# Kernel tuning notes

Hardware: AMD Instinct MI355X
Metric: run time of the kernel (lower is better)

Reference implementation:

```python
import jax, jax.numpy as jnp
import numpy as np

B, T, C, H = 2, 2048, 2048, 16
HD = C // H  # head dim = 128


def setup_inputs() -> dict:
    key = jax.random.key(0)
    k1, k2, k3 = jax.random.split(key, 3)
    x = jax.random.normal(k1, (B, T, C), dtype=jnp.float32)
    # torch Linear stores weight as [out_features, in_features]; y = x @ W.T
    w_attn = jax.random.normal(k2, (3 * C, C), dtype=jnp.float32) * (C ** -0.5)
    w_proj = jax.random.normal(k3, (C, C), dtype=jnp.float32) * (C ** -0.5)
    b_proj = jnp.zeros((C,), dtype=jnp.float32)
    return {"x": x, "w_attn": w_attn, "w_proj": w_proj, "b_proj": b_proj}


def reference(x, w_attn, w_proj, b_proj):
    # c_attn: [B,T,C] -> [B,T,3C], then split into q,k,v
    qkv = jnp.einsum('btc,oc->bto', x, w_attn)
    q, k, v = jnp.split(qkv, 3, axis=-1)
    # [B,T,C] -> [B,H,T,HD]
    q = q.reshape(B, T, H, HD).transpose(0, 2, 1, 3)
    k = k.reshape(B, T, H, HD).transpose(0, 2, 1, 3)
    v = v.reshape(B, T, H, HD).transpose(0, 2, 1, 3)
    scale = 1.0 / jnp.sqrt(jnp.float32(HD))
    att = jnp.einsum('bhqd,bhkd->bhqk', q, k) * scale  # [B,H,T,T]
    causal = jnp.tril(jnp.ones((T, T), dtype=bool))
    att = jnp.where(causal, att, -jnp.inf)
    att = jax.nn.softmax(att, axis=-1)
    # dropout p=0.0 (eval): identity
    y = jnp.einsum('bhqk,bhkd->bhqd', att, v)  # [B,H,T,HD]
    y = y.transpose(0, 2, 1, 3).reshape(B, T, C)
    y = jnp.einsum('btc,oc->bto', y, w_proj) + b_proj
    return y
```

## Files before the change

### kernel.cpp

```cpp
#include <hip/hip_runtime.h>
#include <hip/hip_bf16.h>
#include <stdint.h>
#include <stddef.h>

#define Bn  2
#define Tn  2048
#define Cn  2048
#define Hn  16
#define HDn 128

typedef short short8   __attribute__((ext_vector_type(8)));
typedef short short8_a __attribute__((ext_vector_type(8), may_alias));
typedef unsigned int u32x4_a __attribute__((ext_vector_type(4), may_alias));
typedef unsigned short u16x4_a __attribute__((ext_vector_type(4), may_alias));
typedef unsigned short u16x8_a __attribute__((ext_vector_type(8), may_alias));
typedef float f32x4 __attribute__((ext_vector_type(4)));

typedef __attribute__((address_space(1))) const void av1_t;
typedef __attribute__((address_space(3))) void av3_t;

__device__ inline unsigned short f2b(float f) {
    union { float f; unsigned u; } v; v.f = f;
    unsigned r = v.u + 0x7fffu + ((v.u >> 16) & 1u);
    return (unsigned short)(r >> 16);
}
__device__ inline u16x4_a cvt4_f32_bf16(u32x4_a v) {
    u16x4_a h;
#pragma unroll
    for (int e = 0; e < 4; e++) {
        unsigned u = v[e];
        unsigned r = u + 0x7fffu + ((u >> 16) & 1u);
        h[e] = (unsigned short)(r >> 16);
    }
    return h;
}

__global__ __launch_bounds__(256)
void cvt_kernel(const float* __restrict__ src, unsigned short* __restrict__ dst, int n)
{
    const int i = (blockIdx.x * 256 + threadIdx.x) * 8;
    if (i >= n) return;
    u32x4_a a = *(const u32x4_a*)((const unsigned*)src + i);
    u32x4_a b = *(const u32x4_a*)((const unsigned*)src + i + 4);
    u16x8_a o;
    u16x4_a ha = cvt4_f32_bf16(a), hb = cvt4_f32_bf16(b);
#pragma unroll
    for (int e = 0; e < 4; e++) { o[e] = ha[e]; o[e + 4] = hb[e]; }
    *(u16x8_a*)(dst + i) = o;
}

template<int OUT_F32, int HAS_BIAS>
__global__ __launch_bounds__(256)
void gemm_bb_kernel(const unsigned short* __restrict__ A,
                    const unsigned short* __restrict__ Bm,
                    const float* __restrict__ bias, void* __restrict__ Cv,
                    int M, int N, int K)
{
    __shared__ __align__(16) unsigned short As[128 * 32];
    __shared__ __align__(16) unsigned short Bs[128 * 32];

    const int tid  = threadIdx.x;
    const int lane = tid & 63;
    const int wave = tid >> 6;
    const int quad = lane >> 4;
    const int l15  = lane & 15;
    const int tm = blockIdx.x * 128;
    const int tn = blockIdx.y * 128;
    const int wr = (wave >> 1) * 64;
    const int wc = (wave & 1) * 64;

    const int srow = lane >> 2;
    const int scol = (lane & 3) * 8;

    f32x4 acc[4][4];
#pragma unroll
    for (int i = 0; i < 4; i++)
#pragma unroll
        for (int j = 0; j < 4; j++) acc[i][j] = (f32x4){0.f, 0.f, 0.f, 0.f};

    const int ksteps = K >> 5;
    for (int kt = 0; kt < ksteps; ++kt) {
        const int k0 = kt << 5;
#pragma unroll
        for (int r = 0; r < 2; r++) {
            const int row = (r * 4 + wave) * 16 + srow;
            __builtin_amdgcn_global_load_lds(
                (av1_t*)(A + (size_t)(tm + row) * K + k0 + scol),
                (av3_t*)(&As[row * 32 + scol]), 16, 0, 0);
            __builtin_amdgcn_global_load_lds(
                (av1_t*)(Bm + (size_t)(tn + row) * K + k0 + scol),
                (av3_t*)(&Bs[row * 32 + scol]), 16, 0, 0);
        }
        asm volatile("s_waitcnt vmcnt(0)" ::: "memory");
        __syncthreads();

        short8 af[4], bf[4];
#pragma unroll
        for (int i = 0; i < 4; i++)
            af[i] = (short8)(*(const short8_a*)&As[(wr + i * 16 + l15) * 32 + quad * 8]);
#pragma unroll
        for (int j = 0; j < 4; j++)
            bf[j] = (short8)(*(const short8_a*)&Bs[(wc + j * 16 + l15) * 32 + quad * 8]);
#pragma unroll
        for (int i = 0; i < 4; i++)
#pragma unroll
            for (int j = 0; j < 4; j++)
                acc[i][j] = __builtin_amdgcn_mfma_f32_16x16x32_bf16(af[i], bf[j], acc[i][j], 0, 0, 0);
        __syncthreads();
    }

#pragma unroll
    for (int i = 0; i < 4; i++) {
        const int row = tm + wr + i * 16 + quad * 4;
#pragma unroll
        for (int j = 0; j < 4; j++) {
            const int col = tn + wc + j * 16 + l15;
            const float bv = HAS_BIAS ? bias[col] : 0.0f;
#pragma unroll
            for (int r = 0; r < 4; r++) {
                if (OUT_F32)
                    ((float*)Cv)[(size_t)(row + r) * N + col] = acc[i][j][r] + bv;
                else
                    ((unsigned short*)Cv)[(size_t)(row + r) * N + col] = f2b(acc[i][j][r] + bv);
            }
        }
    }
}

__global__ __launch_bounds__(256)
void gemm_qkv_kernel(const unsigned short* __restrict__ A,
                     const unsigned short* __restrict__ Bm,
                     unsigned short* __restrict__ qout,
                     unsigned short* __restrict__ kvout, int K)
{
    __shared__ __align__(16) unsigned short As[128 * 32];
    __shared__ __align__(16) unsigned short Bs[128 * 32];

    const int tid  = threadIdx.x;
    const int lane = tid & 63;
    const int wave = tid >> 6;
    const int quad = lane >> 4;
    const int l15  = lane & 15;
    const int tm = blockIdx.x * 128;
    const int tn = blockIdx.y * 128;
    const int wr = (wave >> 1) * 64;
    const int wc = (wave & 1) * 64;

    const int srow = lane >> 2;
    const int scol = (lane & 3) * 8;

    f32x4 acc[4][4];
#pragma unroll
    for (int i = 0; i < 4; i++)
#pragma unroll
        for (int j = 0; j < 4; j++) acc[i][j] = (f32x4){0.f, 0.f, 0.f, 0.f};

    const int ksteps = K >> 5;
    for (int kt = 0; kt < ksteps; ++kt) {
        const int k0 = kt << 5;
#pragma unroll
        for (int r = 0; r < 2; r++) {
            const int row = (r * 4 + wave) * 16 + srow;
            __builtin_amdgcn_global_load_lds(
                (av1_t*)(A + (size_t)(tm + row) * K + k0 + scol),
                (av3_t*)(&As[row * 32 + scol]), 16, 0, 0);
            __builtin_amdgcn_global_load_lds(
                (av1_t*)(Bm + (size_t)(tn + row) * K + k0 + scol),
                (av3_t*)(&Bs[row * 32 + scol]), 16, 0, 0);
        }
        asm volatile("s_waitcnt vmcnt(0)" ::: "memory");
        __syncthreads();

        short8 af[4], bf[4];
#pragma unroll
        for (int i = 0; i < 4; i++)
            af[i] = (short8)(*(const short8_a*)&As[(wr + i * 16 + l15) * 32 + quad * 8]);
#pragma unroll
        for (int j = 0; j < 4; j++)
            bf[j] = (short8)(*(const short8_a*)&Bs[(wc + j * 16 + l15) * 32 + quad * 8]);
#pragma unroll
        for (int i = 0; i < 4; i++)
#pragma unroll
            for (int j = 0; j < 4; j++)
                acc[i][j] = __builtin_amdgcn_mfma_f32_16x16x32_bf16(af[i], bf[j], acc[i][j], 0, 0, 0);
        __syncthreads();
    }

    unsigned short* base = (tn < Cn) ? qout : kvout;
    const int cofs = (tn < Cn) ? 0 : Cn;
    const size_t ostr = (tn < Cn) ? Cn : 2 * Cn;
#pragma unroll
    for (int i = 0; i < 4; i++) {
        const int row = tm + wr + i * 16 + quad * 4;
#pragma unroll
        for (int j = 0; j < 4; j++) {
            const int col = tn + wc + j * 16 + l15 - cofs;
#pragma unroll
            for (int r = 0; r < 4; r++)
                base[(size_t)(row + r) * ostr + col] = f2b(acc[i][j][r]);
        }
    }
}

__global__ __launch_bounds__(512, 2)
void attn_kernel(const unsigned short* __restrict__ q,
                 const unsigned short* __restrict__ kv,
                 unsigned short* __restrict__ outp)
{
    __shared__ __align__(16) unsigned short Ks[128 * 136];
    __shared__ __align__(16) unsigned short Vs[128 * 136];
    __shared__ __align__(16) unsigned short Ps[8][16 * 136];

    const int qp   = blockIdx.x;
    const int bh   = blockIdx.y;
    const int b    = bh >> 4;
    const int h    = bh & 15;
    const int tid  = threadIdx.x;
    const int lane = tid & 63;
    const int wave = tid >> 6;
    const int quad = lane >> 4;
    const int l15  = lane & 15;

    short8 ones;
#pragma unroll
    for (int e = 0; e < 8; e++) ones[e] = (short)0x3F80;

    for (int half = 0; half < 2; ++half) {
        const int qt = half ? (15 - qp) : qp;
        const int qrow0 = qt * 128 + wave * 16;

        short8 qf[4];
#pragma unroll
        for (int kk = 0; kk < 4; kk++) {
            const unsigned short* p = q + (size_t)(b * Tn + qrow0 + l15) * Cn
                                      + h * HDn + kk * 32 + quad * 8;
            qf[kk] = (short8)(*(const short8_a*)p);
        }

        float m_i[4], l_i[4];
        f32x4 o_acc[8];
#pragma unroll
        for (int r = 0; r < 4; r++) { m_i[r] = -1e30f; l_i[r] = 0.f; }
#pragma unroll
        for (int jd = 0; jd < 8; jd++) o_acc[jd] = (f32x4){0.f, 0.f, 0.f, 0.f};

        const int ktiles = qt + 1;

        u32x4_a kr[4], vr[4];
        auto preload = [&](int kt2) {
            const int kk0 = kt2 * 128;
#pragma unroll
            for (int rep = 0; rep < 4; ++rep) {
                const int idx  = tid + rep * 512;
                const int krow = idx >> 4;
                const int dg   = (idx & 15) * 8;
                const size_t rb = (size_t)(b * Tn + kk0 + krow) * (2 * Cn) + h * HDn + dg;
                kr[rep] = *(const u32x4_a*)(kv + rb);
                vr[rep] = *(const u32x4_a*)(kv + rb + Cn);
            }
        };
        preload(0);

        for (int kt2 = 0; kt2 < ktiles; ++kt2) {
            const int kk0 = kt2 * 128;
            __syncthreads();
#pragma unroll
            for (int rep = 0; rep < 4; ++rep) {
                const int idx  = tid + rep * 512;
                const int krow = idx >> 4;
                const int l    = idx & 15;
                const int dg   = l * 8;
                *(u32x4_a*)&Ks[krow * 136 + dg] = kr[rep];
                const int pcol = krow ^ ((l & 7) << 3);
                const unsigned short* ve = (const unsigned short*)&vr[rep];
#pragma unroll
                for (int e = 0; e < 8; e++) Vs[(dg + e) * 136 + pcol] = ve[e];
            }
            __syncthreads();
            if (kt2 + 1 < ktiles) preload(kt2 + 1);

            f32x4 s[8];
#pragma unroll
            for (int j = 0; j < 8; j++) s[j] = (f32x4){0.f, 0.f, 0.f, 0.f};
#pragma unroll
            for (int kk = 0; kk < 4; ++kk) {
                short8 kf[8];
#pragma unroll
                for (int j = 0; j < 8; j++)
                    kf[j] = (short8)(*(const short8_a*)&Ks[(j * 16 + l15) * 136 + kk * 32 + quad * 8]);
#pragma unroll
                for (int j = 0; j < 8; j++)
                    s[j] = __builtin_amdgcn_mfma_f32_16x16x32_bf16(qf[kk], kf[j], s[j], 0, 0, 0);
            }

            const bool needmask = (kk0 + 127 > qrow0);
            float alr[4];
#pragma unroll
            for (int r = 0; r < 4; r++) {
                const int qidx = qrow0 + quad * 4 + r;
                float mx = -1e30f;
#pragma unroll
                for (int j = 0; j < 8; j++) {
                    float v = s[j][r] * 0.08838834764831845f;
                    if (needmask) {
                        const int kidx = kk0 + j * 16 + l15;
                        v = (kidx <= qidx) ? v : -1e30f;
                    }
                    s[j][r] = v;
                    mx = fmaxf(mx, v);
                }
#pragma unroll
                for (int off = 1; off < 16; off <<= 1)
                    mx = fmaxf(mx, __shfl_xor(mx, off));
                const float mn = fmaxf(m_i[r], mx);
                alr[r] = __expf(fminf(m_i[r] - mn, 0.f));
                m_i[r] = mn;
#pragma unroll
                for (int j = 0; j < 8; j++) {
                    const float p = __expf(fminf(s[j][r] - mn, 0.f));
                    s[j][r] = p;
                }
#pragma unroll
                for (int jd = 0; jd < 8; jd++) o_acc[jd][r] *= alr[r];
#pragma unroll
                for (int j = 0; j < 8; j++)
                    Ps[wave][(quad * 4 + r) * 136 + j * 16 + l15] = f2b(s[j][r]);
            }
            asm volatile("s_waitcnt lgkmcnt(0)" ::: "memory");

            f32x4 lacc = (f32x4){0.f, 0.f, 0.f, 0.f};
#pragma unroll
            for (int kk2 = 0; kk2 < 4; ++kk2) {
                short8 pf = (short8)(*(const short8_a*)&Ps[wave][l15 * 136 + kk2 * 32 + quad * 8]);
#pragma unroll
                for (int jd = 0; jd < 8; jd++) {
                    const int d = jd * 16 + l15;
                    const int g = (d >> 3) & 7;
                    const int colb = ((4 * kk2 + quad) ^ g) * 8;
                    short8 vf = (short8)(*(const short8_a*)&Vs[d * 136 + colb]);
                    o_acc[jd] = __builtin_amdgcn_mfma_f32_16x16x32_bf16(pf, vf, o_acc[jd], 0, 0, 0);
                }
                lacc = __builtin_amdgcn_mfma_f32_16x16x32_bf16(pf, ones, lacc, 0, 0, 0);
            }
#pragma unroll
            for (int r = 0; r < 4; r++)
                l_i[r] = l_i[r] * alr[r] + lacc[r];
        }

#pragma unroll
        for (int r = 0; r < 4; r++) {
            const float inv = 1.0f / fmaxf(l_i[r], 1e-20f);
            const int trow = qrow0 + quad * 4 + r;
#pragma unroll
            for (int jd = 0; jd < 8; jd++) {
                const int col = h * HDn + jd * 16 + l15;
                outp[(size_t)(b * Tn + trow) * Cn + col] = f2b(o_acc[jd][r] * inv);
            }
        }
    }
}

extern "C" void kernel_launch(void* const* d_in, const int* in_sizes, int n_in,
                              void* d_out, int out_size, void* d_ws, size_t ws_size,
                              hipStream_t stream)
{
    const float* x      = (const float*)d_in[0];
    const float* w_attn = (const float*)d_in[1];
    const float* w_proj = (const float*)d_in[2];
    const float* b_proj = (const float*)d_in[3];
    float* out = (float*)d_out;

    const size_t MiB = 1024 * 1024;
    unsigned short* kvbuf = (unsigned short*)d_out;

    const int nx   = Bn * Tn * Cn;
    const int nwq  = Cn * Cn;
    const int nwkv = 2 * Cn * Cn;
    const int nw全 = 0; (void)nwq;

    if (ws_size >= 56 * MiB) {
        unsigned short* xb   = (unsigned short*)d_ws;
        unsigned short* qbuf = (unsigned short*)((char*)d_ws + 16 * MiB);
        unsigned short* wb   = (unsigned short*)((char*)d_ws + 32 * MiB);
        const int nwa = 3 * Cn * Cn;

        cvt_kernel<<<nx / 8 / 256, 256, 0, stream>>>(x, xb, nx);
        cvt_kernel<<<nwa / 8 / 256, 256, 0, stream>>>(w_attn, wb, nwa);
        gemm_qkv_kernel<<<dim3(32, 48), 256, 0, stream>>>(xb, wb, qbuf, kvbuf, Cn);
        attn_kernel<<<dim3(8, Bn * Hn), 512, 0, stream>>>(qbuf, kvbuf, qbuf);
        cvt_kernel<<<nwq / 8 / 256, 256, 0, stream>>>(w_proj, wb, nwq);
        gemm_bb_kernel<1, 1><<<dim3(32, 16), 256, 0, stream>>>(qbuf, wb, b_proj, out,
                                                               Bn * Tn, Cn, Cn);
    } else {
        unsigned short* xb   = (unsigned short*)d_ws;
        unsigned short* qbuf = (unsigned short*)((char*)d_ws + 16 * MiB);
        unsigned short* wb   = (unsigned short*)((char*)d_ws + 32 * MiB);

        cvt_kernel<<<nx / 8 / 256, 256, 0, stream>>>(x, xb, nx);
        cvt_kernel<<<nwq / 8 / 256, 256, 0, stream>>>(w_attn, wb, nwq);
        gemm_bb_kernel<0, 0><<<dim3(32, 16), 256, 0, stream>>>(xb, wb, nullptr, qbuf,
                                                               Bn * Tn, Cn, Cn);
        cvt_kernel<<<nwkv / 8 / 256, 256, 0, stream>>>(w_attn + (size_t)Cn * Cn, wb, nwkv);
        gemm_bb_kernel<0, 0><<<dim3(32, 32), 256, 0, stream>>>(xb, wb, nullptr, kvbuf,
                                                               Bn * Tn, 2 * Cn, Cn);
        attn_kernel<<<dim3(8, Bn * Hn), 512, 0, stream>>>(qbuf, kvbuf, qbuf);
        cvt_kernel<<<nwq / 8 / 256, 256, 0, stream>>>(w_proj, wb, nwq);
        gemm_bb_kernel<1, 1><<<dim3(32, 16), 256, 0, stream>>>(qbuf, wb, b_proj, out,
                                                               Bn * Tn, Cn, Cn);
    }
}
```

Baseline: 418.6 us.

## Rewrite QKV GEMM with 256x256 tiles, double-buffered LDS pipeline and XCD-aware mapping

Replaces the simple 128x128 QKV GEMM, which waited on every k-step, with a 512-thread 256x256-tile kernel. It double-buffers A/B tiles of K=64 in 64KB of LDS, interleaves global_load_lds prefetches with MFMA phases, and raises wave priority during MFMA. It also XOR-swizzles LDS columns to avoid bank conflicts and remaps block IDs so blocks on each XCD share tiles for L2 reuse. The aim is to hide global memory latency and raise MFMA utilisation, at the cost of a much more complex barrier and waitcnt schedule and higher register pressure.

Result: faster. 406.4 us (-2.9%).

```diff
diff --git a/kernel.cpp b/kernel.cpp
--- a/kernel.cpp
+++ b/kernel.cpp
@@ -127,77 +127,219 @@
     }
 }
 
-__global__ __launch_bounds__(256)
-void gemm_qkv_kernel(const unsigned short* __restrict__ A,
-                     const unsigned short* __restrict__ Bm,
-                     unsigned short* __restrict__ qout,
-                     unsigned short* __restrict__ kvout, int K)
+#define LA0 0
+#define LB0 16384
+#define LA1 32768
+#define LB1 49152
+
+__global__ __launch_bounds__(512, 2)
+void gemm_qkv8_kernel(const unsigned short* __restrict__ A,
+                      const unsigned short* __restrict__ Bm,
+                      unsigned short* __restrict__ qout,
+                      unsigned short* __restrict__ kvout)
 {
-    __shared__ __align__(16) unsigned short As[128 * 32];
-    __shared__ __align__(16) unsigned short Bs[128 * 32];
+    __shared__ __align__(16) unsigned short lds[65536];
 
     const int tid  = threadIdx.x;
     const int lane = tid & 63;
     const int wave = tid >> 6;
     const int quad = lane >> 4;
     const int l15  = lane & 15;
-    const int tm = blockIdx.x * 128;
-    const int tn = blockIdx.y * 128;
-    const int wr = (wave >> 1) * 64;
-    const int wc = (wave & 1) * 64;
-
-    const int srow = lane >> 2;
-    const int scol = (lane & 3) * 8;
-
-    f32x4 acc[4][4];
-#pragma unroll
-    for (int i = 0; i < 4; i++)
+    const int wrow = wave >> 2;
+    const int wcol = wave & 3;
+    const int kswz = (l15 & 4) << 2;
+
+    const int bid = blockIdx.x;
+    const int xcd = bid & 7;
+    const int sl  = bid >> 3;
+    const int bm  = (xcd & 1) * 8 + (sl & 7);
+    const int bn  = (xcd >> 1) * 6 + (sl >> 3);
+    const int tm  = bm * 256;
+    const int tn  = bn * 256;
+
+    const unsigned short* Ab = A  + (size_t)tm * Cn;
+    const unsigned short* Bb = Bm + (size_t)tn * Cn;
+
+    f32x4 acc[8][4];
+#pragma unroll
+    for (int i = 0; i < 8; i++)
 #pragma unroll
         for (int j = 0; j < 4; j++) acc[i][j] = (f32x4){0.f, 0.f, 0.f, 0.f};
 
-    const int ksteps = K >> 5;
-    for (int kt = 0; kt < ksteps; ++kt) {
-        const int k0 = kt << 5;
-#pragma unroll
-        for (int r = 0; r < 2; r++) {
-            const int row = (r * 4 + wave) * 16 + srow;
+    auto stage = [&](const unsigned short* g, int kt, int base, int half) {
+#pragma unroll
+        for (int rr = 0; rr < 2; ++rr) {
+            const int idx = rr * 512 + tid;
+            const int row = idx >> 3;
+            const int ks  = ((idx & 7) * 8) ^ ((row & 4) << 2);
             __builtin_amdgcn_global_load_lds(
-                (av1_t*)(A + (size_t)(tm + row) * K + k0 + scol),
-                (av3_t*)(&As[row * 32 + scol]), 16, 0, 0);
-            __builtin_amdgcn_global_load_lds(
-                (av1_t*)(Bm + (size_t)(tn + row) * K + k0 + scol),
-                (av3_t*)(&Bs[row * 32 + scol]), 16, 0, 0);
-        }
-        asm volatile("s_waitcnt vmcnt(0)" ::: "memory");
-        __syncthreads();
-
-        short8 af[4], bf[4];
-#pragma unroll
-        for (int i = 0; i < 4; i++)
-            af[i] = (short8)(*(const short8_a*)&As[(wr + i * 16 + l15) * 32 + quad * 8]);
-#pragma unroll
-        for (int j = 0; j < 4; j++)
-            bf[j] = (short8)(*(const short8_a*)&Bs[(wc + j * 16 + l15) * 32 + quad * 8]);
-#pragma unroll
-        for (int i = 0; i < 4; i++)
-#pragma unroll
-            for (int j = 0; j < 4; j++)
-                acc[i][j] = __builtin_amdgcn_mfma_f32_16x16x32_bf16(af[i], bf[j], acc[i][j], 0, 0, 0);
-        __syncthreads();
-    }
-
-    unsigned short* base = (tn < Cn) ? qout : kvout;
-    const int cofs = (tn < Cn) ? 0 : Cn;
+                (av1_t*)(g + (size_t)(half * 128 + row) * Cn + kt * 64 + ks),
+                (av3_t*)(lds + base + half * 8192 + idx * 8), 16, 0, 0);
+        }
+    };
+    auto lda = [&](int base, int i, int ks) -> short8 {
+        return (short8)(*(const short8_a*)&lds[base + (wrow * 128 + i * 16 + l15) * 64
+                                               + ((ks * 32 + quad * 8) ^ kswz)]);
+    };
+    auto ldb = [&](int base, int j, int ks) -> short8 {
+        return (short8)(*(const short8_a*)&lds[base + (wcol * 64 + j * 16 + l15) * 64
+                                               + ((ks * 32 + quad * 8) ^ kswz)]);
+    };
+
+    stage(Ab, 0, LA0, 0); stage(Ab, 0, LA0, 1);
+    stage(Bb, 0, LB0, 0); stage(Bb, 0, LB0, 1);
+    stage(Ab, 1, LA1, 0); stage(Ab, 1, LA1, 1);
+    asm volatile("s_waitcnt vmcnt(4)" ::: "memory");
+    __builtin_amdgcn_s_barrier();
+
+    const int nt = Cn / 64;
+    for (int t = 0; t < nt; t += 2) {
+        const bool tail = (t + 2 >= nt);
+        short8 af[8][2], bf[2][2];
+
+#pragma unroll
+        for (int i = 0; i < 4; i++) { af[i][0] = lda(LA0, i, 0); af[i][1] = lda(LA0, i, 1); }
+#pragma unroll
+        for (int j = 0; j < 2; j++) { bf[j][0] = ldb(LB0, j, 0); bf[j][1] = ldb(LB0, j, 1); }
+        stage(Bb, t + 1, LB1, 0);
+        __builtin_amdgcn_s_barrier();
+        asm volatile("s_waitcnt lgkmcnt(0)" ::: "memory");
+        __builtin_amdgcn_s_setprio(1);
+#pragma unroll
+        for (int ks = 0; ks < 2; ks++)
+#pragma unroll
+            for (int i = 0; i < 4; i++)
+#pragma unroll
+                for (int j = 0; j < 2; j++)
+                    acc[i][j] = __builtin_amdgcn_mfma_f32_16x16x32_bf16(af[i][ks], bf[j][ks], acc[i][j], 0, 0, 0);
+        __builtin_amdgcn_s_setprio(0);
+        __builtin_amdgcn_s_barrier();
+
+#pragma unroll
+        for (int i = 4; i < 8; i++) { af[i][0] = lda(LA0, i, 0); af[i][1] = lda(LA0, i, 1); }
+        stage(Bb, t + 1, LB1, 1);
+        __builtin_amdgcn_s_barrier();
+        asm volatile("s_waitcnt lgkmcnt(0)" ::: "memory");
+        __builtin_amdgcn_s_setprio(1);
+#pragma unroll
+        for (int ks = 0; ks < 2; ks++)
+#pragma unroll
+            for (int i = 4; i < 8; i++)
+#pragma unroll
+                for (int j = 0; j < 2; j++)
+                    acc[i][j] = __builtin_amdgcn_mfma_f32_16x16x32_bf16(af[i][ks], bf[j][ks], acc[i][j], 0, 0, 0);
+        __builtin_amdgcn_s_setprio(0);
+        __builtin_amdgcn_s_barrier();
+
+#pragma unroll
+        for (int j = 0; j < 2; j++) { bf[j][0] = ldb(LB0, 2 + j, 0); bf[j][1] = ldb(LB0, 2 + j, 1); }
+        if (!tail) stage(Ab, t + 2, LA0, 0);
+        __builtin_amdgcn_s_barrier();
+        asm volatile("s_waitcnt lgkmcnt(0)" ::: "memory");
+        __builtin_amdgcn_s_setprio(1);
+#pragma unroll
+        for (int ks = 0; ks < 2; ks++)
+#pragma unroll
+            for (int i = 0; i < 4; i++)
+#pragma unroll
+                for (int j = 0; j < 2; j++)
+                    acc[i][2 + j] = __builtin_amdgcn_mfma_f32_16x16x32_bf16(af[i][ks], bf[j][ks], acc[i][2 + j], 0, 0, 0);
+        __builtin_amdgcn_s_setprio(0);
+        __builtin_amdgcn_s_barrier();
+
+        if (!tail) stage(Ab, t + 2, LA0, 1);
+        __builtin_amdgcn_s_barrier();
+        __builtin_amdgcn_s_setprio(1);
+#pragma unroll
+        for (int ks = 0; ks < 2; ks++)
+#pragma unroll
+            for (int i = 4; i < 8; i++)
+#pragma unroll
+                for (int j = 0; j < 2; j++)
+                    acc[i][2 + j] = __builtin_amdgcn_mfma_f32_16x16x32_bf16(af[i][ks], bf[j][ks], acc[i][2 + j], 0, 0, 0);
+        __builtin_amdgcn_s_setprio(0);
+        if (tail) asm volatile("s_waitcnt vmcnt(0)" ::: "memory");
+        else      asm volatile("s_waitcnt vmcnt(4)" ::: "memory");
+        __builtin_amdgcn_s_barrier();
+
+#pragma unroll
+        for (int i = 0; i < 4; i++) { af[i][0] = lda(LA1, i, 0); af[i][1] = lda(LA1, i, 1); }
+#pragma unroll
+        for (int j = 0; j < 2; j++) { bf[j][0] = ldb(LB1, j, 0); bf[j][1] = ldb(LB1, j, 1); }
+        if (!tail) stage(Bb, t + 2, LB0, 0);
+        __builtin_amdgcn_s_barrier();
+        asm volatile("s_waitcnt lgkmcnt(0)" ::: "memory");
+        __builtin_amdgcn_s_setprio(1);
+#pragma unroll
+        for (int ks = 0; ks < 2; ks++)
+#pragma unroll
+            for (int i = 0; i < 4; i++)
+#pragma unroll
+                for (int j = 0; j < 2; j++)
+                    acc[i][j] = __builtin_amdgcn_mfma_f32_16x16x32_bf16(af[i][ks], bf[j][ks], acc[i][j], 0, 0, 0);
+        __builtin_amdgcn_s_setprio(0);
+        __builtin_amdgcn_s_barrier();
+
+#pragma unroll
+        for (int i = 4; i < 8; i++) { af[i][0] = lda(LA1, i, 0); af[i][1] = lda(LA1, i, 1); }
+        if (!tail) stage(Bb, t + 2, LB0, 1);
+        __builtin_amdgcn_s_barrier();
+        asm volatile("s_waitcnt lgkmcnt(0)" ::: "memory");
+        __builtin_amdgcn_s_setprio(1);
+#pragma unroll
+        for (int ks = 0; ks < 2; ks++)
+#pragma unroll
+            for (int i = 4; i < 8; i++)
+#pragma unroll
+                for (int j = 0; j < 2; j++)
+                    acc[i][j] = __builtin_amdgcn_mfma_f32_16x16x32_bf16(af[i][ks], bf[j][ks], acc[i][j], 0, 0, 0);
+        __builtin_amdgcn_s_setprio(0);
+        __builtin_amdgcn_s_barrier();
+
+#pragma unroll
+        for (int j = 0; j < 2; j++) { bf[j][0] = ldb(LB1, 2 + j, 0); bf[j][1] = ldb(LB1, 2 + j, 1); }
+        if (!tail) stage(Ab, t + 3, LA1, 0);
+        __builtin_amdgcn_s_barrier();
+        asm volatile("s_waitcnt lgkmcnt(0)" ::: "memory");
+        __builtin_amdgcn_s_setprio(1);
+#pragma unroll
+        for (int ks = 0; ks < 2; ks++)
+#pragma unroll
+            for (int i = 0; i < 4; i++)
+#pragma unroll
+                for (int j = 0; j < 2; j++)
+                    acc[i][2 + j] = __builtin_amdgcn_mfma_f32_16x16x32_bf16(af[i][ks], bf[j][ks], acc[i][2 + j], 0, 0, 0);
+        __builtin_amdgcn_s_setprio(0);
+        __builtin_amdgcn_s_barrier();
+
+        if (!tail) stage(Ab, t + 3, LA1, 1);
+        __builtin_amdgcn_s_barrier();
+        __builtin_amdgcn_s_setprio(1);
+#pragma unroll
+        for (int ks = 0; ks < 2; ks++)
+#pragma unroll
+            for (int i = 4; i < 8; i++)
+#pragma unroll
+                for (int j = 0; j < 2; j++)
+                    acc[i][2 + j] = __builtin_amdgcn_mfma_f32_16x16x32_bf16(af[i][ks], bf[j][ks], acc[i][2 + j], 0, 0, 0);
+        __builtin_amdgcn_s_setprio(0);
+        if (tail) asm volatile("s_waitcnt vmcnt(0)" ::: "memory");
+        else      asm volatile("s_waitcnt vmcnt(4)" ::: "memory");
+        __builtin_amdgcn_s_barrier();
+    }
+
+    unsigned short* obase = (tn < Cn) ? qout : kvout;
+    const int cofs   = (tn < Cn) ? 0 : Cn;
     const size_t ostr = (tn < Cn) ? Cn : 2 * Cn;
 #pragma unroll
-    for (int i = 0; i < 4; i++) {
-        const int row = tm + wr + i * 16 + quad * 4;
+    for (int i = 0; i < 8; i++) {
+        const int row = tm + wrow * 128 + i * 16 + quad * 4;
 #pragma unroll
         for (int j = 0; j < 4; j++) {
-            const int col = tn + wc + j * 16 + l15 - cofs;
+            const int col = tn + wcol * 64 + j * 16 + l15 - cofs;
 #pragma unroll
             for (int r = 0; r < 4; r++)
-                base[(size_t)(row + r) * ostr + col] = f2b(acc[i][j][r]);
+                obase[(size_t)(row + r) * ostr + col] = f2b(acc[i][j][r]);
         }
     }
 }
@@ -376,7 +518,6 @@
     const int nx   = Bn * Tn * Cn;
     const int nwq  = Cn * Cn;
     const int nwkv = 2 * Cn * Cn;
-    const int nw全 = 0; (void)nwq;
 
     if (ws_size >= 56 * MiB) {
         unsigned short* xb   = (unsigned short*)d_ws;
@@ -386,7 +527,7 @@
 
         cvt_kernel<<<nx / 8 / 256, 256, 0, stream>>>(x, xb, nx);
         cvt_kernel<<<nwa / 8 / 256, 256, 0, stream>>>(w_attn, wb, nwa);
-        gemm_qkv_kernel<<<dim3(32, 48), 256, 0, stream>>>(xb, wb, qbuf, kvbuf, Cn);
+        gemm_qkv8_kernel<<<dim3(384), 512, 0, stream>>>(xb, wb, qbuf, kvbuf);
         attn_kernel<<<dim3(8, Bn * Hn), 512, 0, stream>>>(qbuf, kvbuf, qbuf);
         cvt_kernel<<<nwq / 8 / 256, 256, 0, stream>>>(w_proj, wb, nwq);
         gemm_bb_kernel<1, 1><<<dim3(32, 16), 256, 0, stream>>>(qbuf, wb, b_proj, out,
```
